# Performance work log

Measured on AMD Instinct MI355X. Metric: run time of the kernel, lower is better.

## Reference

```python
import jax, jax.numpy as jnp
import numpy as np

NUM_REL = 20000
NUM_EDGES = 640000
DIM_IN = 128
DIM_OUT = 128
NUM_HEAD = 8
DIM_HID = DIM_OUT // NUM_HEAD
NUM_BIN = 10
NEG_SLOPE = 0.2


def leaky_relu(x):
    return jnp.where(x >= 0, x, NEG_SLOPE * x)


def setup_inputs() -> dict:
    key = jax.random.key(0)
    ks = jax.random.split(key, 8)
    emb_rel = jax.random.normal(ks[0], (NUM_REL, DIM_IN), dtype=jnp.float32)
    head = jax.random.randint(ks[1], (NUM_EDGES, 1), 0, NUM_REL)
    tail = jax.random.randint(ks[2], (NUM_EDGES, 1), 0, NUM_REL)
    bins = jax.random.randint(ks[3], (NUM_EDGES, 1), 0, NUM_BIN)
    relation_triplets = jnp.concatenate([head, tail, bins], axis=-1).astype(jnp.int64)
    # xavier-normal-ish init
    attn_proj_w = jax.random.normal(ks[4], (DIM_OUT, 2 * DIM_IN), dtype=jnp.float32) * (2.0 / np.sqrt(2 * DIM_IN + DIM_OUT))
    attn_proj_b = jnp.zeros((DIM_OUT,), dtype=jnp.float32)
    attn_bin = jax.random.normal(ks[5], (NUM_BIN, NUM_HEAD, 1), dtype=jnp.float32) * 0.3
    attn_vec = jax.random.normal(ks[6], (1, NUM_HEAD, DIM_HID), dtype=jnp.float32) * (2.0 / np.sqrt(NUM_HEAD * DIM_HID))
    aggr_proj_w = jax.random.normal(ks[7], (DIM_OUT, DIM_IN), dtype=jnp.float32) * (2.0 / np.sqrt(DIM_IN + DIM_OUT))
    aggr_proj_b = jnp.zeros((DIM_OUT,), dtype=jnp.float32)
    return {"emb_rel": emb_rel, "relation_triplets": relation_triplets,
            "attn_proj_w": attn_proj_w, "attn_proj_b": attn_proj_b,
            "attn_bin": attn_bin, "attn_vec": attn_vec,
            "aggr_proj_w": aggr_proj_w, "aggr_proj_b": aggr_proj_b}


def reference(emb_rel, relation_triplets, attn_proj_w, attn_proj_b, attn_bin, attn_vec, aggr_proj_w, aggr_proj_b):
    num_rel = emb_rel.shape[0]
    head = relation_triplets[..., 0]
    tail = relation_triplets[..., 1]
    bins = relation_triplets[..., 2]
    # edge gather + concat: [E, 2*dim_in]
    concat = jnp.concatenate([emb_rel[head], emb_rel[tail]], axis=-1)
    proj = concat @ attn_proj_w.T + attn_proj_b  # [E, dim_out]
    proj = leaky_relu(proj).reshape(-1, NUM_HEAD, DIM_HID)
    attn_raw = (proj * attn_vec).sum(axis=-1, keepdims=True) + leaky_relu(attn_bin[bins])  # [E,H,1]
    # per-head-relation segment softmax over edges grouped by head index
    seg_max = jax.ops.segment_max(attn_raw, head, num_segments=num_rel)  # [R,H,1]
    attn_val = jnp.exp(attn_raw - seg_max[head])
    seg_sum = jax.ops.segment_sum(attn_val, head, num_segments=num_rel)  # [R,H,1]
    beta = attn_val / (seg_sum[head] + 1e-16)
    msg = (emb_rel[tail] @ aggr_proj_w.T + aggr_proj_b).reshape(-1, NUM_HEAD, DIM_HID)
    out = jax.ops.segment_sum(beta * msg, head, num_segments=num_rel)  # [R,H,Dh]
    return out.reshape(num_rel, -1)
```

## Files before the change

kernel.cpp:

```cpp
#include <hip/hip_runtime.h>
#include <hip/hip_bf16.h>
#include <cstdint>
#include <cstddef>

#define NUM_REL    20000
#define NUM_EDGES  640000
#define DIM        128
#define NUM_HEAD   8
#define DIM_HID    16
#define NUM_BIN    10
#define CAP        128
#define PROJ_BLKS  471
#define SC_BLKS    2500

using u16 = unsigned short;
using u32 = unsigned int;
typedef __attribute__((ext_vector_type(8))) short bf16x8;
typedef __attribute__((ext_vector_type(4))) float f32x4;

__device__ __forceinline__ float b2f(u16 u) { return __uint_as_float(((u32)u) << 16); }
__device__ __forceinline__ float lo2f(u32 u) { return __uint_as_float(u << 16); }
__device__ __forceinline__ float hi2f(u32 u) { return __uint_as_float(u & 0xffff0000u); }
__device__ __forceinline__ float lrelu(float x) { return fmaxf(x, 0.2f * x); }
__device__ __forceinline__ int clampi(int v, int hi) { return v < 0 ? 0 : (v > hi ? hi : v); }
__device__ __forceinline__ float ldf(const void* p, int f32m, int i)
{ return f32m ? ((const float*)p)[i] : b2f(((const u16*)p)[i]); }
__device__ __forceinline__ u16 f2b(float x)
{ u32 u = __float_as_uint(x); u += 0x7fffu + ((u >> 16) & 1u); return (u16)(u >> 16); }
__device__ __forceinline__ u32 pk2(float a, float b)
{ return (u32)f2b(a) | ((u32)f2b(b) << 16); }

__device__ __forceinline__ void detect_flags(const int* __restrict__ trip,
                                             const u16* __restrict__ emb,
                                             int* sF, int tid)
{
    if (tid < 64) {
        bool odd_zero = (trip[2 * tid + 1] == 0) && (trip[2 * tid + 129] == 0);
        unsigned long long m1 = __ballot(odd_zero);
        int ex = (emb[2 * tid] >> 7) & 0xFF;
        bool inr = (ex >= 110) && (ex <= 136);
        unsigned long long m2 = __ballot(inr);
        if (tid == 0) {
            sF[0] = (~m1 == 0ull) ? 1 : 0;
            sF[1] = (__popcll(m2) >= 32) ? 0 : 1;
        }
    }
    __syncthreads();
}

__global__ __launch_bounds__(256) void k_projscatter(
    const void* __restrict__ emb, const int* __restrict__ trip,
    const void* __restrict__ w_attn, const void* __restrict__ w_aggr,
    const void* __restrict__ b_attn, const void* __restrict__ b_aggr,
    float* __restrict__ A, u16* __restrict__ Bb, u16* __restrict__ Mb,
    int* __restrict__ cnt, int* __restrict__ bucket)
{
    __shared__ u16 sW[128 * 128];
    __shared__ float sBias[128];
    __shared__ int sF[2];

    const int tid = threadIdx.x;
    detect_flags(trip, (const u16*)emb, sF, tid);
    const int is64 = sF[0], f32m = sF[1];

    if (blockIdx.x >= PROJ_BLKS) {
        int e = (blockIdx.x - PROJ_BLKS) * 256 + tid;
        if (e < NUM_EDGES) {
            int h, t, b;
            if (is64) {
                int2 hh = *(const int2*)(trip + 6 * e);
                int2 tt = *(const int2*)(trip + 6 * e + 2);
                int2 bb = *(const int2*)(trip + 6 * e + 4);
                h = hh.x; t = tt.x; b = bb.x;
            } else {
                h = trip[3 * e]; t = trip[3 * e + 1]; b = trip[3 * e + 2];
            }
            h = clampi(h, NUM_REL - 1);
            t = clampi(t, NUM_REL - 1);
            b = clampi(b, NUM_BIN - 1);
            int pos = atomicAdd(&cnt[h], 1);
            if (pos < CAP) bucket[h * CAP + pos] = t | (b << 20);
        }
        return;
    }

    const int mt = blockIdx.x / 3, nt = blockIdx.x % 3;
    const int r0 = mt * 128;

    if (tid < 128)
        sBias[tid] = (nt == 0) ? 0.f : ldf((nt == 1) ? b_attn : b_aggr, f32m, tid);

    {
        const void* wsrc = (nt == 2) ? w_aggr : w_attn;
        const int stride = (nt == 2) ? 128 : 256;
        const int koff   = (nt == 1) ? 128 : 0;
        if (f32m) {
            const float* src = (const float*)wsrc;
            #pragma unroll
            for (int i = 0; i < 16; ++i) {
                int f = i * 256 + tid;
                int row = f >> 5, pos = f & 31;
                float4 x = ((const float4*)(src + (size_t)row * stride + koff))[pos];
                int chunk = (pos >> 1) ^ (row & 15);
                *(uint2*)&sW[row * 128 + chunk * 8 + (pos & 1) * 4] =
                    make_uint2(pk2(x.x, x.y), pk2(x.z, x.w));
            }
        } else {
            const u16* src = (const u16*)wsrc;
            #pragma unroll
            for (int i = 0; i < 8; ++i) {
                int f = i * 256 + tid;
                int row = f >> 4, pos = f & 15;
                uint4 x = ((const uint4*)(src + (size_t)row * stride + koff))[pos];
                int chunk = pos ^ (row & 15);
                *(uint4*)&sW[row * 128 + chunk * 8] = x;
            }
        }
    }
    __syncthreads();

    const int lane = tid & 63, wid = tid >> 6;
    const int wm = (wid >> 1) * 64, wn = (wid & 1) * 64;
    const int ln15 = lane & 15, q = lane >> 4;

    int arow[4];
    #pragma unroll
    for (int mi = 0; mi < 4; ++mi) {
        int g = r0 + wm + mi * 16 + ln15;
        arow[mi] = (g < NUM_REL) ? g : (NUM_REL - 1);
    }

    f32x4 acc[4][4] = {};
    #pragma unroll
    for (int kk = 0; kk < 4; ++kk) {
        const int cbase = kk * 4 + q;
        const int kc = cbase * 8;
        bf16x8 a[4], b[4];
        #pragma unroll
        for (int mi = 0; mi < 4; ++mi) {
            if (f32m) {
                const float* er = (const float*)emb + (size_t)arow[mi] * DIM + kc;
                float4 x0 = *(const float4*)er;
                float4 x1 = *(const float4*)(er + 4);
                union { bf16x8 v; u32 u[4]; } cv;
                cv.u[0] = pk2(x0.x, x0.y); cv.u[1] = pk2(x0.z, x0.w);
                cv.u[2] = pk2(x1.x, x1.y); cv.u[3] = pk2(x1.z, x1.w);
                a[mi] = cv.v;
            } else {
                a[mi] = *(const bf16x8*)((const u16*)emb + (size_t)arow[mi] * DIM + kc);
            }
        }
        #pragma unroll
        for (int ni = 0; ni < 4; ++ni) {
            int n = wn + ni * 16 + ln15;
            int c = cbase ^ ln15;
            b[ni] = *(const bf16x8*)&sW[n * 128 + c * 8];
        }
        #pragma unroll
        for (int mi = 0; mi < 4; ++mi)
            #pragma unroll
            for (int ni = 0; ni < 4; ++ni)
                acc[mi][ni] = __builtin_amdgcn_mfma_f32_16x16x32_bf16(
                    a[mi], b[ni], acc[mi][ni], 0, 0, 0);
    }

    #pragma unroll
    for (int mi = 0; mi < 4; ++mi) {
        #pragma unroll
        for (int reg = 0; reg < 4; ++reg) {
            int g = r0 + wm + mi * 16 + q * 4 + reg;
            if (g < NUM_REL) {
                #pragma unroll
                for (int ni = 0; ni < 4; ++ni) {
                    int c = wn + ni * 16 + ln15;
                    float v = acc[mi][ni][reg] + sBias[c];
                    size_t o = (size_t)g * DIM + c;
                    if (nt == 0)      A[o]  = v;
                    else if (nt == 1) Bb[o] = f2b(v);
                    else              Mb[o] = f2b(v);
                }
            }
        }
    }
}

__global__ __launch_bounds__(256, 6) void k_segment(
    const float* __restrict__ A, const u16* __restrict__ Bb,
    const u16* __restrict__ Mb, const void* __restrict__ attn_bin,
    const void* __restrict__ attn_vec, const int* __restrict__ cnt,
    const int* __restrict__ bucket, const int* __restrict__ trip,
    const void* __restrict__ emb, void* __restrict__ out)
{
    __shared__ float sAr[4][DIM];
    __shared__ float sVec[DIM];
    __shared__ float sBin[NUM_BIN * NUM_HEAD];
    __shared__ int sF[2];

    const int tid  = threadIdx.x;
    detect_flags(trip, (const u16*)emb, sF, tid);
    const int f32m = sF[1];

    const int wid  = tid >> 6, lane = tid & 63;
    const int r = blockIdx.x * 4 + wid;
    int nE = cnt[r]; if (nE > CAP) nE = CAP;
    const int* __restrict__ bk = bucket + r * CAP;

    {
        const float2* ap = (const float2*)(A + (size_t)r * DIM);
        float2 a2 = ap[lane];
        sAr[wid][2 * lane] = a2.x; sAr[wid][2 * lane + 1] = a2.y;
    }
    if (tid < DIM) sVec[tid] = ldf(attn_vec, f32m, tid);
    else if (tid < DIM + NUM_BIN * NUM_HEAD)
        sBin[tid - DIM] = lrelu(ldf(attn_bin, f32m, tid - DIM));
    __syncthreads();

    if (nE == 0) {
        if (f32m) ((float2*)out)[(size_t)r * 64 + lane] = make_float2(0.f, 0.f);
        else      ((u32*)out)[(size_t)r * 64 + lane] = 0;
        return;
    }

    const int el = lane >> 3, hd = lane & 7;
    const int ah = lane >> 3;

    float av[16], vv[16];
    {
        const float4* pA = (const float4*)(&sAr[wid][hd * DIM_HID]);
        const float4* pV = (const float4*)(&sVec[hd * DIM_HID]);
        #pragma unroll
        for (int i = 0; i < 4; ++i) {
            float4 a4 = pA[i], v4 = pV[i];
            av[4*i+0]=a4.x; av[4*i+1]=a4.y; av[4*i+2]=a4.z; av[4*i+3]=a4.w;
            vv[4*i+0]=v4.x; vv[4*i+1]=v4.y; vv[4*i+2]=v4.z; vv[4*i+3]=v4.w;
        }
    }

    const u16* __restrict__ Mbl = Mb + 2 * lane;

    int tb = (el < nE) ? bk[el] : 0;
    int t  = tb & 0xFFFFF;
    uint4 q0, q1;
    {
        const uint4* Bt = (const uint4*)(Bb + (size_t)t * DIM) + hd * 2;
        q0 = Bt[0]; q1 = Bt[1];
    }

    float l = 0.f;
    float ax0 = 0.f, ax1 = 0.f, ay0 = 0.f, ay1 = 0.f;

    for (int base = 0; base < nE; base += 8) {
        u32 mm[8];
        #pragma unroll
        for (int k = 0; k < 8; ++k) {
            int tk = __shfl(t, k * 8);
            mm[k] = *(const u32*)(Mbl + (size_t)tk * DIM);
        }
        const int bsel = (tb >> 20) & 0xF;

        int e_n  = base + 8 + el;
        int tb_n = (e_n < nE) ? bk[e_n] : 0;
        int t_n  = tb_n & 0xFFFFF;
        uint4 q0n, q1n;
        {
            const uint4* Btn = (const uint4*)(Bb + (size_t)t_n * DIM) + hd * 2;
            q0n = Btn[0]; q1n = Btn[1];
        }

        float s0 = sBin[bsel * NUM_HEAD + hd];
        s0 = fmaf(lrelu(av[0]  + lo2f(q0.x)), vv[0],  s0);
        float s1 = lrelu(av[1] + hi2f(q0.x)) * vv[1];
        float s2 = lrelu(av[2] + lo2f(q0.y)) * vv[2];
        float s3 = lrelu(av[3] + hi2f(q0.y)) * vv[3];
        s0 = fmaf(lrelu(av[4]  + lo2f(q0.z)), vv[4],  s0);
        s1 = fmaf(lrelu(av[5]  + hi2f(q0.z)), vv[5],  s1);
        s2 = fmaf(lrelu(av[6]  + lo2f(q0.w)), vv[6],  s2);
        s3 = fmaf(lrelu(av[7]  + hi2f(q0.w)), vv[7],  s3);
        s0 = fmaf(lrelu(av[8]  + lo2f(q1.x)), vv[8],  s0);
        s1 = fmaf(lrelu(av[9]  + hi2f(q1.x)), vv[9],  s1);
        s2 = fmaf(lrelu(av[10] + lo2f(q1.y)), vv[10], s2);
        s3 = fmaf(lrelu(av[11] + hi2f(q1.y)), vv[11], s3);
        s0 = fmaf(lrelu(av[12] + lo2f(q1.z)), vv[12], s0);
        s1 = fmaf(lrelu(av[13] + hi2f(q1.z)), vv[13], s1);
        s2 = fmaf(lrelu(av[14] + lo2f(q1.w)), vv[14], s2);
        s3 = fmaf(lrelu(av[15] + hi2f(q1.w)), vv[15], s3);
        float s = (s0 + s1) + (s2 + s3);
        s = fminf(fmaxf(s, -60.f), 60.f);
        float p = ((base + el) < nE) ? __expf(s) : 0.f;
        l += p;

        #pragma unroll
        for (int k = 0; k < 8; ++k) {
            float v = __shfl(p, k * 8 + ah);
            if (k & 1) {
                ax1 = fmaf(v, lo2f(mm[k]), ax1);
                ay1 = fmaf(v, hi2f(mm[k]), ay1);
            } else {
                ax0 = fmaf(v, lo2f(mm[k]), ax0);
                ay0 = fmaf(v, hi2f(mm[k]), ay0);
            }
        }

        tb = tb_n; t = t_n; q0 = q0n; q1 = q1n;
    }

    float accx = ax0 + ax1, accy = ay0 + ay1;

    float lt = l + __shfl_xor(l, 8);
    lt += __shfl_xor(lt, 16);
    lt += __shfl_xor(lt, 32);
    float lA = __shfl(lt, ah);
    float inv = 1.0f / (lA + 1e-16f);
    float o0 = accx * inv, o1 = accy * inv;
    if (f32m) {
        ((float2*)out)[(size_t)r * 64 + lane] = make_float2(o0, o1);
    } else {
        u32 pk = (u32)f2b(o0) | ((u32)f2b(o1) << 16);
        ((u32*)out)[(size_t)r * 64 + lane] = pk;
    }
}

extern "C" void kernel_launch(void* const* d_in, const int* in_sizes, int n_in,
                              void* d_out, int out_size, void* d_ws, size_t ws_size,
                              hipStream_t stream)
{
    (void)in_sizes; (void)n_in; (void)out_size; (void)ws_size;
    const void* emb      = d_in[0];
    const int*  trip     = (const int*)d_in[1];
    const void* w_attn   = d_in[2];
    const void* b_attn   = d_in[3];
    const void* attn_bin = d_in[4];
    const void* attn_vec = d_in[5];
    const void* w_aggr   = d_in[6];
    const void* b_aggr   = d_in[7];

    char* p = (char*)d_ws;
    float* A      = (float*)p; p += (size_t)NUM_REL * DIM * 4;
    u16*   Bb     = (u16*)p;   p += (size_t)NUM_REL * DIM * 2;
    u16*   Mb     = (u16*)p;   p += (size_t)NUM_REL * DIM * 2;
    int*   bucket = (int*)p;   p += (size_t)NUM_REL * CAP * 4;
    int*   cnt    = (int*)p;   p += (size_t)NUM_REL * 4;

    hipMemsetAsync(cnt, 0, NUM_REL * sizeof(int), stream);
    k_projscatter<<<PROJ_BLKS + SC_BLKS, 256, 0, stream>>>(
        emb, trip, w_attn, w_aggr, b_attn, b_aggr, A, Bb, Mb, cnt, bucket);
    k_segment<<<NUM_REL / 4, 256, 0, stream>>>(A, Bb, Mb, attn_bin, attn_vec,
                                               cnt, bucket, trip, emb, d_out);
}
```

Before: 179.4 us.

## Pad atomic counters, halve GEMM weight smem, double per-iteration edges in segment loop

Several changes at once. Per-relation counters are padded to 64-byte stride so atomics on different heads avoid the same cache line, and each scatter thread now handles two edges. The projection GEMM stages weights in two 64-wide K halves, halving LDS use to raise occupancy. The segment-softmax loop processes 16 edges per iteration with two independent gather/score chains for more memory-level parallelism, with launch bounds lowered to allow the extra registers. Risks are lower occupancy in k_segment, an extra barrier in the GEMM, and a larger memset.

```diff
diff --git a/kernel.cpp b/kernel.cpp
--- a/kernel.cpp
+++ b/kernel.cpp
@@ -10,8 +10,9 @@
 #define DIM_HID    16
 #define NUM_BIN    10
 #define CAP        128
+#define CNT_STR    16
 #define PROJ_BLKS  471
-#define SC_BLKS    2500
+#define SC_BLKS    1250
 
 using u16 = unsigned short;
 using u32 = unsigned int;
@@ -55,7 +56,7 @@
     float* __restrict__ A, u16* __restrict__ Bb, u16* __restrict__ Mb,
     int* __restrict__ cnt, int* __restrict__ bucket)
 {
-    __shared__ u16 sW[128 * 128];
+    __shared__ u16 sW[128 * 64];
     __shared__ float sBias[128];
     __shared__ int sF[2];
 
@@ -64,23 +65,28 @@
     const int is64 = sF[0], f32m = sF[1];
 
     if (blockIdx.x >= PROJ_BLKS) {
-        int e = (blockIdx.x - PROJ_BLKS) * 256 + tid;
-        if (e < NUM_EDGES) {
-            int h, t, b;
-            if (is64) {
-                int2 hh = *(const int2*)(trip + 6 * e);
-                int2 tt = *(const int2*)(trip + 6 * e + 2);
-                int2 bb = *(const int2*)(trip + 6 * e + 4);
-                h = hh.x; t = tt.x; b = bb.x;
-            } else {
-                h = trip[3 * e]; t = trip[3 * e + 1]; b = trip[3 * e + 2];
-            }
-            h = clampi(h, NUM_REL - 1);
-            t = clampi(t, NUM_REL - 1);
-            b = clampi(b, NUM_BIN - 1);
-            int pos = atomicAdd(&cnt[h], 1);
-            if (pos < CAP) bucket[h * CAP + pos] = t | (b << 20);
-        }
+        int e0 = (blockIdx.x - PROJ_BLKS) * 512 + tid;
+        int e1 = e0 + 256;
+        int h0, t0, b0, h1, t1, b1;
+        if (is64) {
+            int2 ha = *(const int2*)(trip + 6 * e0);
+            int2 ta = *(const int2*)(trip + 6 * e0 + 2);
+            int2 ba = *(const int2*)(trip + 6 * e0 + 4);
+            int2 hb = *(const int2*)(trip + 6 * e1);
+            int2 tb = *(const int2*)(trip + 6 * e1 + 2);
+            int2 bb = *(const int2*)(trip + 6 * e1 + 4);
+            h0 = ha.x; t0 = ta.x; b0 = ba.x;
+            h1 = hb.x; t1 = tb.x; b1 = bb.x;
+        } else {
+            h0 = trip[3 * e0]; t0 = trip[3 * e0 + 1]; b0 = trip[3 * e0 + 2];
+            h1 = trip[3 * e1]; t1 = trip[3 * e1 + 1]; b1 = trip[3 * e1 + 2];
+        }
+        h0 = clampi(h0, NUM_REL - 1); t0 = clampi(t0, NUM_REL - 1); b0 = clampi(b0, NUM_BIN - 1);
+        h1 = clampi(h1, NUM_REL - 1); t1 = clampi(t1, NUM_REL - 1); b1 = clampi(b1, NUM_BIN - 1);
+        int p0 = atomicAdd(&cnt[h0 * CNT_STR], 1);
+        int p1 = atomicAdd(&cnt[h1 * CNT_STR], 1);
+        if (p0 < CAP) bucket[h0 * CAP + p0] = t0 | (b0 << 20);
+        if (p1 < CAP) bucket[h1 * CAP + p1] = t1 | (b1 << 20);
         return;
     }
 
@@ -90,34 +96,9 @@
     if (tid < 128)
         sBias[tid] = (nt == 0) ? 0.f : ldf((nt == 1) ? b_attn : b_aggr, f32m, tid);
 
-    {
-        const void* wsrc = (nt == 2) ? w_aggr : w_attn;
-        const int stride = (nt == 2) ? 128 : 256;
-        const int koff   = (nt == 1) ? 128 : 0;
-        if (f32m) {
-            const float* src = (const float*)wsrc;
-            #pragma unroll
-            for (int i = 0; i < 16; ++i) {
-                int f = i * 256 + tid;
-                int row = f >> 5, pos = f & 31;
-                float4 x = ((const float4*)(src + (size_t)row * stride + koff))[pos];
-                int chunk = (pos >> 1) ^ (row & 15);
-                *(uint2*)&sW[row * 128 + chunk * 8 + (pos & 1) * 4] =
-                    make_uint2(pk2(x.x, x.y), pk2(x.z, x.w));
-            }
-        } else {
-            const u16* src = (const u16*)wsrc;
-            #pragma unroll
-            for (int i = 0; i < 8; ++i) {
-                int f = i * 256 + tid;
-                int row = f >> 4, pos = f & 15;
-                uint4 x = ((const uint4*)(src + (size_t)row * stride + koff))[pos];
-                int chunk = pos ^ (row & 15);
-                *(uint4*)&sW[row * 128 + chunk * 8] = x;
-            }
-        }
-    }
-    __syncthreads();
+    const void* wsrc = (nt == 2) ? w_aggr : w_attn;
+    const int stride = (nt == 2) ? 128 : 256;
+    const int koff   = (nt == 1) ? 128 : 0;
 
     const int lane = tid & 63, wid = tid >> 6;
     const int wm = (wid >> 1) * 64, wn = (wid & 1) * 64;
@@ -132,36 +113,66 @@
 
     f32x4 acc[4][4] = {};
     #pragma unroll
-    for (int kk = 0; kk < 4; ++kk) {
-        const int cbase = kk * 4 + q;
-        const int kc = cbase * 8;
-        bf16x8 a[4], b[4];
-        #pragma unroll
-        for (int mi = 0; mi < 4; ++mi) {
-            if (f32m) {
-                const float* er = (const float*)emb + (size_t)arow[mi] * DIM + kc;
-                float4 x0 = *(const float4*)er;
-                float4 x1 = *(const float4*)(er + 4);
-                union { bf16x8 v; u32 u[4]; } cv;
-                cv.u[0] = pk2(x0.x, x0.y); cv.u[1] = pk2(x0.z, x0.w);
-                cv.u[2] = pk2(x1.x, x1.y); cv.u[3] = pk2(x1.z, x1.w);
-                a[mi] = cv.v;
-            } else {
-                a[mi] = *(const bf16x8*)((const u16*)emb + (size_t)arow[mi] * DIM + kc);
-            }
-        }
-        #pragma unroll
-        for (int ni = 0; ni < 4; ++ni) {
-            int n = wn + ni * 16 + ln15;
-            int c = cbase ^ ln15;
-            b[ni] = *(const bf16x8*)&sW[n * 128 + c * 8];
-        }
-        #pragma unroll
-        for (int mi = 0; mi < 4; ++mi)
-            #pragma unroll
-            for (int ni = 0; ni < 4; ++ni)
-                acc[mi][ni] = __builtin_amdgcn_mfma_f32_16x16x32_bf16(
-                    a[mi], b[ni], acc[mi][ni], 0, 0, 0);
+    for (int kh = 0; kh < 2; ++kh) {
+        if (kh) __syncthreads();
+        if (f32m) {
+            const float* src = (const float*)wsrc;
+            #pragma unroll
+            for (int i = 0; i < 8; ++i) {
+                int f = i * 256 + tid;
+                int row = f >> 4, pos = f & 15;
+                const float* rp = src + (size_t)row * stride + koff + kh * 64;
+                float4 x = ((const float4*)rp)[pos];
+                int chunk = (pos >> 1) ^ (row & 7);
+                *(uint2*)&sW[row * 64 + chunk * 8 + (pos & 1) * 4] =
+                    make_uint2(pk2(x.x, x.y), pk2(x.z, x.w));
+            }
+        } else {
+            const u16* src = (const u16*)wsrc;
+            #pragma unroll
+            for (int i = 0; i < 4; ++i) {
+                int f = i * 256 + tid;
+                int row = f >> 3, pos = f & 7;
+                const u16* rp = src + (size_t)row * stride + koff + kh * 64;
+                uint4 x = ((const uint4*)rp)[pos];
+                int chunk = pos ^ (row & 7);
+                *(uint4*)&sW[row * 64 + chunk * 8] = x;
+            }
+        }
+        __syncthreads();
+
+        #pragma unroll
+        for (int k2 = 0; k2 < 2; ++k2) {
+            const int kkg = kh * 2 + k2;
+            const int kc = (kkg * 4 + q) * 8;
+            const int cl = (k2 * 4 + q) ^ (ln15 & 7);
+            bf16x8 a[4], b[4];
+            #pragma unroll
+            for (int mi = 0; mi < 4; ++mi) {
+                if (f32m) {
+                    const float* er = (const float*)emb + (size_t)arow[mi] * DIM + kc;
+                    float4 x0 = *(const float4*)er;
+                    float4 x1 = *(const float4*)(er + 4);
+                    union { bf16x8 v; u32 u[4]; } cv;
+                    cv.u[0] = pk2(x0.x, x0.y); cv.u[1] = pk2(x0.z, x0.w);
+                    cv.u[2] = pk2(x1.x, x1.y); cv.u[3] = pk2(x1.z, x1.w);
+                    a[mi] = cv.v;
+                } else {
+                    a[mi] = *(const bf16x8*)((const u16*)emb + (size_t)arow[mi] * DIM + kc);
+                }
+            }
+            #pragma unroll
+            for (int ni = 0; ni < 4; ++ni) {
+                int n = wn + ni * 16 + ln15;
+                b[ni] = *(const bf16x8*)&sW[n * 64 + cl * 8];
+            }
+            #pragma unroll
+            for (int mi = 0; mi < 4; ++mi)
+                #pragma unroll
+                for (int ni = 0; ni < 4; ++ni)
+                    acc[mi][ni] = __builtin_amdgcn_mfma_f32_16x16x32_bf16(
+                        a[mi], b[ni], acc[mi][ni], 0, 0, 0);
+        }
     }
 
     #pragma unroll
@@ -184,7 +195,7 @@
     }
 }
 
-__global__ __launch_bounds__(256, 6) void k_segment(
+__global__ __launch_bounds__(256, 4) void k_segment(
     const float* __restrict__ A, const u16* __restrict__ Bb,
     const u16* __restrict__ Mb, const void* __restrict__ attn_bin,
     const void* __restrict__ attn_vec, const int* __restrict__ cnt,
@@ -202,7 +213,7 @@
 
     const int wid  = tid >> 6, lane = tid & 63;
     const int r = blockIdx.x * 4 + wid;
-    int nE = cnt[r]; if (nE > CAP) nE = CAP;
+    int nE = cnt[r * CNT_STR]; if (nE > CAP) nE = CAP;
     const int* __restrict__ bk = bucket + r * CAP;
 
     {
@@ -238,70 +249,105 @@
 
     const u16* __restrict__ Mbl = Mb + 2 * lane;
 
-    int tb = (el < nE) ? bk[el] : 0;
-    int t  = tb & 0xFFFFF;
-    uint4 q0, q1;
+    int tba = (el      < nE) ? bk[el]     : 0;
+    int tbb = (8 + el  < nE) ? bk[8 + el] : 0;
+    int ia = tba & 0xFFFFF, ib = tbb & 0xFFFFF;
+    uint4 q0a, q1a, q0b, q1b;
     {
-        const uint4* Bt = (const uint4*)(Bb + (size_t)t * DIM) + hd * 2;
-        q0 = Bt[0]; q1 = Bt[1];
+        const uint4* Ba = (const uint4*)(Bb + (size_t)ia * DIM) + hd * 2;
+        const uint4* Bc = (const uint4*)(Bb + (size_t)ib * DIM) + hd * 2;
+        q0a = Ba[0]; q1a = Ba[1];
+        q0b = Bc[0]; q1b = Bc[1];
     }
 
     float l = 0.f;
     float ax0 = 0.f, ax1 = 0.f, ay0 = 0.f, ay1 = 0.f;
 
-    for (int base = 0; base < nE; base += 8) {
-        u32 mm[8];
+    for (int base = 0; base < nE; base += 16) {
+        u32 mm[16];
         #pragma unroll
         for (int k = 0; k < 8; ++k) {
-            int tk = __shfl(t, k * 8);
+            int tk = __shfl(ia, k * 8);
             mm[k] = *(const u32*)(Mbl + (size_t)tk * DIM);
         }
-        const int bsel = (tb >> 20) & 0xF;
-
-        int e_n  = base + 8 + el;
-        int tb_n = (e_n < nE) ? bk[e_n] : 0;
-        int t_n  = tb_n & 0xFFFFF;
-        uint4 q0n, q1n;
+        #pragma unroll
+        for (int k = 0; k < 8; ++k) {
+            int tk = __shfl(ib, k * 8);
+            mm[8 + k] = *(const u32*)(Mbl + (size_t)tk * DIM);
+        }
+        const int bsa = (tba >> 20) & 0xF;
+        const int bsb = (tbb >> 20) & 0xF;
+
+        int ea_n  = base + 16 + el;
+        int eb_n  = base + 24 + el;
+        int tba_n = (ea_n < nE) ? bk[ea_n] : 0;
+        int tbb_n = (eb_n < nE) ? bk[eb_n] : 0;
+        int ia_n  = tba_n & 0xFFFFF, ib_n = tbb_n & 0xFFFFF;
+        uint4 q0an, q1an, q0bn, q1bn;
         {
-            const uint4* Btn = (const uint4*)(Bb + (size_t)t_n * DIM) + hd * 2;
-            q0n = Btn[0]; q1n = Btn[1];
-        }
-
-        float s0 = sBin[bsel * NUM_HEAD + hd];
-        s0 = fmaf(lrelu(av[0]  + lo2f(q0.x)), vv[0],  s0);
-        float s1 = lrelu(av[1] + hi2f(q0.x)) * vv[1];
-        float s2 = lrelu(av[2] + lo2f(q0.y)) * vv[2];
-        float s3 = lrelu(av[3] + hi2f(q0.y)) * vv[3];
-        s0 = fmaf(lrelu(av[4]  + lo2f(q0.z)), vv[4],  s0);
-        s1 = fmaf(lrelu(av[5]  + hi2f(q0.z)), vv[5],  s1);
-        s2 = fmaf(lrelu(av[6]  + lo2f(q0.w)), vv[6],  s2);
-        s3 = fmaf(lrelu(av[7]  + hi2f(q0.w)), vv[7],  s3);
-        s0 = fmaf(lrelu(av[8]  + lo2f(q1.x)), vv[8],  s0);
-        s1 = fmaf(lrelu(av[9]  + hi2f(q1.x)), vv[9],  s1);
-        s2 = fmaf(lrelu(av[10] + lo2f(q1.y)), vv[10], s2);
-        s3 = fmaf(lrelu(av[11] + hi2f(q1.y)), vv[11], s3);
-        s0 = fmaf(lrelu(av[12] + lo2f(q1.z)), vv[12], s0);
-        s1 = fmaf(lrelu(av[13] + hi2f(q1.z)), vv[13], s1);
-        s2 = fmaf(lrelu(av[14] + lo2f(q1.w)), vv[14], s2);
-        s3 = fmaf(lrelu(av[15] + hi2f(q1.w)), vv[15], s3);
-        float s = (s0 + s1) + (s2 + s3);
-        s = fminf(fmaxf(s, -60.f), 60.f);
-        float p = ((base + el) < nE) ? __expf(s) : 0.f;
-        l += p;
+            const uint4* Ban = (const uint4*)(Bb + (size_t)ia_n * DIM) + hd * 2;
+            const uint4* Bcn = (const uint4*)(Bb + (size_t)ib_n * DIM) + hd * 2;
+            q0an = Ban[0]; q1an = Ban[1];
+            q0bn = Bcn[0]; q1bn = Bcn[1];
+        }
+
+        float sa0 = sBin[bsa * NUM_HEAD + hd];
+        float sb0 = sBin[bsb * NUM_HEAD + hd];
+        sa0 = fmaf(lrelu(av[0]  + lo2f(q0a.x)), vv[0],  sa0);
+        sb0 = fmaf(lrelu(av[0]  + lo2f(q0b.x)), vv[0],  sb0);
+        float sa1 = lrelu(av[1] + hi2f(q0a.x)) * vv[1];
+        float sb1 = lrelu(av[1] + hi2f(q0b.x)) * vv[1];
+        float sa2 = lrelu(av[2] + lo2f(q0a.y)) * vv[2];
+        float sb2 = lrelu(av[2] + lo2f(q0b.y)) * vv[2];
+        float sa3 = lrelu(av[3] + hi2f(q0a.y)) * vv[3];
+        float sb3 = lrelu(av[3] + hi2f(q0b.y)) * vv[3];
+        sa0 = fmaf(lrelu(av[4]  + lo2f(q0a.z)), vv[4],  sa0);
+        sb0 = fmaf(lrelu(av[4]  + lo2f(q0b.z)), vv[4],  sb0);
+        sa1 = fmaf(lrelu(av[5]  + hi2f(q0a.z)), vv[5],  sa1);
+        sb1 = fmaf(lrelu(av[5]  + hi2f(q0b.z)), vv[5],  sb1);
+        sa2 = fmaf(lrelu(av[6]  + lo2f(q0a.w)), vv[6],  sa2);
+        sb2 = fmaf(lrelu(av[6]  + lo2f(q0b.w)), vv[6],  sb2);
+        sa3 = fmaf(lrelu(av[7]  + hi2f(q0a.w)), vv[7],  sa3);
+        sb3 = fmaf(lrelu(av[7]  + hi2f(q0b.w)), vv[7],  sb3);
+        sa0 = fmaf(lrelu(av[8]  + lo2f(q1a.x)), vv[8],  sa0);
+        sb0 = fmaf(lrelu(av[8]  + lo2f(q1b.x)), vv[8],  sb0);
+        sa1 = fmaf(lrelu(av[9]  + hi2f(q1a.x)), vv[9],  sa1);
+        sb1 = fmaf(lrelu(av[9]  + hi2f(q1b.x)), vv[9],  sb1);
+        sa2 = fmaf(lrelu(av[10] + lo2f(q1a.y)), vv[10], sa2);
+        sb2 = fmaf(lrelu(av[10] + lo2f(q1b.y)), vv[10], sb2);
+        sa3 = fmaf(lrelu(av[11] + hi2f(q1a.y)), vv[11], sa3);
+        sb3 = fmaf(lrelu(av[11] + hi2f(q1b.y)), vv[11], sb3);
+        sa0 = fmaf(lrelu(av[12] + lo2f(q1a.z)), vv[12], sa0);
+        sb0 = fmaf(lrelu(av[12] + lo2f(q1b.z)), vv[12], sb0);
+        sa1 = fmaf(lrelu(av[13] + hi2f(q1a.z)), vv[13], sa1);
+        sb1 = fmaf(lrelu(av[13] + hi2f(q1b.z)), vv[13], sb1);
+        sa2 = fmaf(lrelu(av[14] + lo2f(q1a.w)), vv[14], sa2);
+        sb2 = fmaf(lrelu(av[14] + lo2f(q1b.w)), vv[14], sb2);
+        sa3 = fmaf(lrelu(av[15] + hi2f(q1a.w)), vv[15], sa3);
+        sb3 = fmaf(lrelu(av[15] + hi2f(q1b.w)), vv[15], sb3);
+        float sa = (sa0 + sa1) + (sa2 + sa3);
+        float sb = (sb0 + sb1) + (sb2 + sb3);
+        sa = fminf(fmaxf(sa, -60.f), 60.f);
+        sb = fminf(fmaxf(sb, -60.f), 60.f);
+        float pa = ((base + el)     < nE) ? __expf(sa) : 0.f;
+        float pb = ((base + 8 + el) < nE) ? __expf(sb) : 0.f;
+        l += pa + pb;
 
         #pragma unroll
         for (int k = 0; k < 8; ++k) {
-            float v = __shfl(p, k * 8 + ah);
-            if (k & 1) {
-                ax1 = fmaf(v, lo2f(mm[k]), ax1);
-                ay1 = fmaf(v, hi2f(mm[k]), ay1);
-            } else {
-                ax0 = fmaf(v, lo2f(mm[k]), ax0);
-                ay0 = fmaf(v, hi2f(mm[k]), ay0);
-            }
-        }
-
-        tb = tb_n; t = t_n; q0 = q0n; q1 = q1n;
+            float v = __shfl(pa, k * 8 + ah);
+            if (k & 1) { ax1 = fmaf(v, lo2f(mm[k]), ax1); ay1 = fmaf(v, hi2f(mm[k]), ay1); }
+            else       { ax0 = fmaf(v, lo2f(mm[k]), ax0); ay0 = fmaf(v, hi2f(mm[k]), ay0); }
+        }
+        #pragma unroll
+        for (int k = 0; k < 8; ++k) {
+            float v = __shfl(pb, k * 8 + ah);
+            if (k & 1) { ax1 = fmaf(v, lo2f(mm[8+k]), ax1); ay1 = fmaf(v, hi2f(mm[8+k]), ay1); }
+            else       { ax0 = fmaf(v, lo2f(mm[8+k]), ax0); ay0 = fmaf(v, hi2f(mm[8+k]), ay0); }
+        }
+
+        tba = tba_n; tbb = tbb_n; ia = ia_n; ib = ib_n;
+        q0a = q0an; q1a = q1an; q0b = q0bn; q1b = q1bn;
     }
 
     float accx = ax0 + ax1, accy = ay0 + ay1;
@@ -339,9 +385,9 @@
     u16*   Bb     = (u16*)p;   p += (size_t)NUM_REL * DIM * 2;
     u16*   Mb     = (u16*)p;   p += (size_t)NUM_REL * DIM * 2;
     int*   bucket = (int*)p;   p += (size_t)NUM_REL * CAP * 4;
-    int*   cnt    = (int*)p;   p += (size_t)NUM_REL * 4;
-
-    hipMemsetAsync(cnt, 0, NUM_REL * sizeof(int), stream);
+    int*   cnt    = (int*)p;   p += (size_t)NUM_REL * CNT_STR * 4;
+
+    hipMemsetAsync(cnt, 0, (size_t)NUM_REL * CNT_STR * sizeof(int), stream);
     k_projscatter<<<PROJ_BLKS + SC_BLKS, 256, 0, stream>>>(
         emb, trip, w_attn, w_aggr, b_attn, b_aggr, A, Bb, Mb, cnt, bucket);
     k_segment<<<NUM_REL / 4, 256, 0, stream>>>(A, Bb, Mb, attn_bin, attn_vec,
```

After: 162.9 us. 9.2% less time.
